# Performance work log

Measured on AMD Instinct MI355X. Metric: run time of the kernel, lower is better.

## Reference

```python
import jax, jax.numpy as jnp
import numpy as np

N = 50000      # nodes
E = 800000     # edges (before self-loops)
F_IN = 16      # input features
H = 8          # heads
C = 16         # out channels per head
HID = H * C    # 128
NEG_SLOPE = 0.2


def setup_inputs() -> dict:
    key = jax.random.key(0)
    ks = jax.random.split(key, 16)
    x = jax.random.normal(ks[0], (N, F_IN), jnp.float32)
    edge_index = jax.random.randint(ks[1], (2, E), 0, N, dtype=jnp.int64)

    def lin(k, fan_in, fan_out):
        return jax.random.normal(k, (fan_in, fan_out), jnp.float32) / np.sqrt(fan_in)

    def att(k):
        return jax.random.normal(k, (H, C), jnp.float32) * 0.1

    return {
        "x": x, "edge_index": edge_index,
        "W1": lin(ks[2], F_IN, HID), "a1_src": att(ks[3]), "a1_dst": att(ks[4]), "b1": jnp.zeros((HID,), jnp.float32),
        "W2": lin(ks[5], HID, HID),  "a2_src": att(ks[6]), "a2_dst": att(ks[7]), "b2": jnp.zeros((HID,), jnp.float32),
        "W3": lin(ks[8], HID, HID),  "a3_src": att(ks[9]), "a3_dst": att(ks[10]), "b3": jnp.zeros((HID,), jnp.float32),
        "fc_w": lin(ks[11], HID, 1), "fc_b": jnp.zeros((1,), jnp.float32),
    }


def gat_layer(x, src, dst, W, a_src, a_dst, b):
    # x: [N, Fin] -> h: [N, H, C]
    h = (x @ W).reshape(-1, H, C)
    al_src = jnp.einsum('nhc,hc->nh', h, a_src)  # [N, H]
    al_dst = jnp.einsum('nhc,hc->nh', h, a_dst)  # [N, H]
    e = jax.nn.leaky_relu(al_src[src] + al_dst[dst], NEG_SLOPE)  # [Etot, H]
    # segment softmax over destination node (self-loops guarantee nonempty segments)
    m = jax.ops.segment_max(e, dst, num_segments=N)
    p = jnp.exp(e - m[dst])
    s = jax.ops.segment_sum(p, dst, num_segments=N)
    alpha = p / s[dst]                                            # [Etot, H]
    out = jax.ops.segment_sum(h[src] * alpha[:, :, None], dst, num_segments=N)  # [N, H, C]
    return out.reshape(-1, HID) + b


def reference(x, edge_index, W1, a1_src, a1_dst, b1, W2, a2_src, a2_dst, b2,
              W3, a3_src, a3_dst, b3, fc_w, fc_b):
    loops = jnp.arange(N, dtype=edge_index.dtype)
    src = jnp.concatenate([edge_index[0], loops])  # add self-loops (PyG default)
    dst = jnp.concatenate([edge_index[1], loops])
    h = jax.nn.elu(gat_layer(x, src, dst, W1, a1_src, a1_dst, b1))
    h = jax.nn.elu(gat_layer(h, src, dst, W2, a2_src, a2_dst, b2))
    h = jax.nn.elu(gat_layer(h, src, dst, W3, a3_src, a3_dst, b3))
    return h @ fc_w + fc_b  # [N, 1]
```

## Files before the change

kernel.cpp:

```cpp
#include <hip/hip_runtime.h>
#include <math.h>

#define N_NODES 50000
#define E_EDGES 800000
#define F_IN 16
#define H_HEADS 8
#define HID 128
#define NEG_SLOPE 0.2f
#define N_PART 8
#define PART_SZ ((N_NODES + N_PART - 1) / N_PART)

typedef __attribute__((ext_vector_type(8))) short short8v;
typedef __attribute__((ext_vector_type(4))) float f32x4;

__device__ __forceinline__ unsigned short f2bf(float f) {
    unsigned u = __float_as_uint(f);
    return (unsigned short)((u + 0x7FFFu + ((u >> 16) & 1u)) >> 16);
}

__global__ void setup(int* __restrict__ deg, const float* __restrict__ W2,
                      unsigned short* __restrict__ Wt2, const float* __restrict__ W3,
                      unsigned short* __restrict__ Wt3) {
    int t = blockIdx.x * 256 + threadIdx.x;
    if (t < N_NODES) deg[t] = 0;
    if (t < HID * HID) {
        int col = t >> 7, k = t & 127;
        Wt2[t] = f2bf(W2[k * HID + col]);
        Wt3[t] = f2bf(W3[k * HID + col]);
    }
}


__global__ void hist_dst(const int* __restrict__ ei, int* __restrict__ deg) {
    int part = blockIdx.x & 7;
    int e = (blockIdx.x >> 3) * 256 + threadIdx.x;
    if (e >= E_EDGES) return;
    int d = ei[E_EDGES + e];
    if (d / PART_SZ == part) atomicAdd(&deg[d], 1);
}

__global__ void scan1(const int* __restrict__ deg, int* __restrict__ rowptr,
                      int* __restrict__ partial) {
    __shared__ int tmp[256];
    int tid = threadIdx.x;
    int t = blockIdx.x * 256 + tid;
    int v = (t < N_NODES) ? deg[t] : 0;
    tmp[tid] = v;
    __syncthreads();
    for (int off = 1; off < 256; off <<= 1) {
        int add = (tid >= off) ? tmp[tid - off] : 0;
        __syncthreads();
        tmp[tid] += add;
        __syncthreads();
    }
    if (t < N_NODES) rowptr[t] = tmp[tid] - v;
    if (tid == 255) partial[blockIdx.x] = tmp[255];
}

__global__ void scan2(int* __restrict__ partial, int nblk) {
    __shared__ int tmp[256];
    int tid = threadIdx.x;
    int v = (tid < nblk) ? partial[tid] : 0;
    tmp[tid] = v;
    __syncthreads();
    for (int off = 1; off < 256; off <<= 1) {
        int add = (tid >= off) ? tmp[tid - off] : 0;
        __syncthreads();
        tmp[tid] += add;
        __syncthreads();
    }
    if (tid < nblk) partial[tid] = tmp[tid] - v;
}

__global__ void scan3(int* __restrict__ rowptr, const int* __restrict__ partial,
                      int* __restrict__ deg) {
    int t = blockIdx.x * 256 + threadIdx.x;
    if (t < N_NODES) {
        rowptr[t] += partial[blockIdx.x];
        deg[t] = 0;
    }
    if (t == 0) rowptr[N_NODES] = E_EDGES;
}

__global__ void scatter(const int* __restrict__ ei, const int* __restrict__ rowptr,
                        int* __restrict__ cursor, int* __restrict__ csr) {
    int part = blockIdx.x & 7;
    int e = (blockIdx.x >> 3) * 256 + threadIdx.x;
    if (e >= E_EDGES) return;
    int d = ei[E_EDGES + e];
    if (d / PART_SZ != part) return;
    int s = ei[e];
    int pos = atomicAdd(&cursor[d], 1);
    csr[rowptr[d] + pos] = s;
}

template <int K>
__global__ __launch_bounds__(256) void gemm_tile(const float* __restrict__ A,
                                                 const float* __restrict__ W,
                                                 unsigned short* __restrict__ C,
                                                 const float* __restrict__ a_src,
                                                 const float* __restrict__ a_dst,
                                                 float* __restrict__ alS,
                                                 float* __restrict__ alD, int M) {
    constexpr int BK = (K < 32) ? K : 32;
    constexpr int BKQ = BK / 4;
    __shared__ float sA[BK][128];
    __shared__ float sW[BK][128];
    int tid = threadIdx.x;
    int tx = tid & 15, ty = tid >> 4;
    int row0 = blockIdx.x * 128;
    float acc[8][8] = {};

    for (int kc = 0; kc < K; kc += BK) {
#pragma unroll
        for (int f = tid; f < 128 * BKQ; f += 256) {
            int r = f / BKQ, kq = f % BKQ;
            int gr = row0 + r;
            float4 v = (gr < M) ? *(const float4*)(A + (size_t)gr * K + kc + kq * 4)
                                : make_float4(0.f, 0.f, 0.f, 0.f);
            sA[kq * 4 + 0][r] = v.x;
            sA[kq * 4 + 1][r] = v.y;
            sA[kq * 4 + 2][r] = v.z;
            sA[kq * 4 + 3][r] = v.w;
        }
#pragma unroll
        for (int f = tid; f < BK * 32; f += 256) {
            int kr = f / 32, cq = f % 32;
            *(float4*)(&sW[kr][cq * 4]) =
                *(const float4*)(W + (size_t)(kc + kr) * 128 + cq * 4);
        }
        __syncthreads();
#pragma unroll
        for (int k = 0; k < BK; k++) {
            float4 a0 = *(const float4*)(&sA[k][ty * 8]);
            float4 a1 = *(const float4*)(&sA[k][ty * 8 + 4]);
            float4 w0 = *(const float4*)(&sW[k][tx * 4]);
            float4 w1 = *(const float4*)(&sW[k][64 + tx * 4]);
            float av[8] = {a0.x, a0.y, a0.z, a0.w, a1.x, a1.y, a1.z, a1.w};
            float wv[8] = {w0.x, w0.y, w0.z, w0.w, w1.x, w1.y, w1.z, w1.w};
#pragma unroll
            for (int i = 0; i < 8; i++)
#pragma unroll
                for (int j = 0; j < 8; j++) acc[i][j] += av[i] * wv[j];
        }
        __syncthreads();
    }

    int hd0 = tx >> 2, co = (tx & 3) * 4;
    float4 as0 = *(const float4*)(a_src + hd0 * 16 + co);
    float4 as1 = *(const float4*)(a_src + (4 + hd0) * 16 + co);
    float4 ad0 = *(const float4*)(a_dst + hd0 * 16 + co);
    float4 ad1 = *(const float4*)(a_dst + (4 + hd0) * 16 + co);

#pragma unroll
    for (int i = 0; i < 8; i++) {
        int gr = row0 + ty * 8 + i;
        if (gr >= M) break;
        float4 c0 = make_float4(acc[i][0], acc[i][1], acc[i][2], acc[i][3]);
        float4 c1 = make_float4(acc[i][4], acc[i][5], acc[i][6], acc[i][7]);
        ushort4 p0 = {f2bf(c0.x), f2bf(c0.y), f2bf(c0.z), f2bf(c0.w)};
        ushort4 p1 = {f2bf(c1.x), f2bf(c1.y), f2bf(c1.z), f2bf(c1.w)};
        *(ushort4*)(C + (size_t)gr * 128 + tx * 4) = p0;
        *(ushort4*)(C + (size_t)gr * 128 + 64 + tx * 4) = p1;
        float s1a = c0.x * as0.x + c0.y * as0.y + c0.z * as0.z + c0.w * as0.w;
        float s1b = c1.x * as1.x + c1.y * as1.y + c1.z * as1.z + c1.w * as1.w;
        float s2a = c0.x * ad0.x + c0.y * ad0.y + c0.z * ad0.z + c0.w * ad0.w;
        float s2b = c1.x * ad1.x + c1.y * ad1.y + c1.z * ad1.z + c1.w * ad1.w;
        s1a += __shfl_xor(s1a, 1); s1a += __shfl_xor(s1a, 2);
        s1b += __shfl_xor(s1b, 1); s1b += __shfl_xor(s1b, 2);
        s2a += __shfl_xor(s2a, 1); s2a += __shfl_xor(s2a, 2);
        s2b += __shfl_xor(s2b, 1); s2b += __shfl_xor(s2b, 2);
        if ((tx & 3) == 0) {
            alS[gr * 8 + hd0] = s1a;
            alS[gr * 8 + 4 + hd0] = s1b;
            alD[gr * 8 + hd0] = s2a;
            alD[gr * 8 + 4 + hd0] = s2b;
        }
    }
}

__global__ __launch_bounds__(256) void gemm_mfma(const unsigned short* __restrict__ Abf,
                                                 const unsigned short* __restrict__ Wt,
                                                 unsigned short* __restrict__ C, int M) {
    __shared__ unsigned short sA[HID * HID];
    __shared__ unsigned short sW[HID * HID];
    char* sAb = (char*)sA;
    char* sWb = (char*)sW;
    int tid = threadIdx.x;
    int row0 = blockIdx.x * 128;

#pragma unroll
    for (int i = 0; i < 8; i++) {
        int f = tid + i * 256;
        int r = f >> 4, c = f & 15;
        int dst = r * 256 + ((c * 16) ^ ((r & 7) << 4));
        int gr = row0 + r;
        short8v va = {0, 0, 0, 0, 0, 0, 0, 0};
        if (gr < M) va = *(const short8v*)(Abf + (size_t)gr * HID + c * 8);
        *(short8v*)(sAb + dst) = va;
        *(short8v*)(sWb + dst) = *(const short8v*)(Wt + r * HID + c * 8);
    }
    __syncthreads();

    int lane = tid & 63;
    int wv = tid >> 6;
    int l15 = lane & 15, kg = lane >> 4;
    f32x4 acc[2][8];
#pragma unroll
    for (int a = 0; a < 2; a++)
#pragma unroll
        for (int j = 0; j < 8; j++) acc[a][j] = f32x4{0.f, 0.f, 0.f, 0.f};

    int rowA0 = wv * 32 + l15;
    int rowA1 = rowA0 + 16;
    int xr = (rowA0 & 7) << 4;

#pragma unroll
    for (int kt = 0; kt < 4; kt++) {
        int kb = kt * 64 + kg * 16;
        short8v a0 = *(const short8v*)(sAb + rowA0 * 256 + (kb ^ xr));
        short8v a1 = *(const short8v*)(sAb + rowA1 * 256 + (kb ^ xr));
#pragma unroll
        for (int j = 0; j < 8; j++) {
            int colr = j * 16 + l15;
            short8v b = *(const short8v*)(sWb + colr * 256 + (kb ^ ((colr & 7) << 4)));
            acc[0][j] = __builtin_amdgcn_mfma_f32_16x16x32_bf16(a0, b, acc[0][j], 0, 0, 0);
            acc[1][j] = __builtin_amdgcn_mfma_f32_16x16x32_bf16(a1, b, acc[1][j], 0, 0, 0);
        }
    }

#pragma unroll
    for (int a = 0; a < 2; a++) {
        int rbase = row0 + wv * 32 + a * 16 + kg * 4;
#pragma unroll
        for (int j = 0; j < 8; j++) {
            int col = j * 16 + l15;
#pragma unroll
            for (int reg = 0; reg < 4; reg++) {
                int gr = rbase + reg;
                if (gr < M) C[(size_t)gr * HID + col] = f2bf(acc[a][j][reg]);
            }
        }
    }
}

__global__ void calc_al(const unsigned short* __restrict__ hbf,
                        const float* __restrict__ a_src, const float* __restrict__ a_dst,
                        float* __restrict__ alS, float* __restrict__ alD) {
    int t = blockIdx.x * 256 + threadIdx.x;
    if (t >= N_NODES * H_HEADS) return;
    int n = t >> 3, hd = t & 7;
    const unsigned short* hr = hbf + (size_t)n * HID + hd * 16;
    float s1 = 0.f, s2 = 0.f;
#pragma unroll
    for (int c = 0; c < 16; c += 2) {
        unsigned g = *(const unsigned*)(hr + c);
        float v0 = __uint_as_float(g << 16);
        float v1 = __uint_as_float(g & 0xFFFF0000u);
        s1 += v0 * a_src[hd * 16 + c] + v1 * a_src[hd * 16 + c + 1];
        s2 += v0 * a_dst[hd * 16 + c] + v1 * a_dst[hd * 16 + c + 1];
    }
    alS[t] = s1;
    alD[t] = s2;
}

template <int MODE>
__global__ void node_agg(const int* __restrict__ rowptr, const int* __restrict__ csr,
                         const float* __restrict__ alS, const float* __restrict__ alD,
                         const unsigned short* __restrict__ hbf, const float* __restrict__ b,
                         unsigned short* __restrict__ h_out, const float* __restrict__ fcw,
                         const float* __restrict__ fcb, float* __restrict__ fco) {
    int node = blockIdx.x * 4 + (threadIdx.x >> 6);
    if (node >= N_NODES) return;
    int lane = threadIdx.x & 63;
    int row0 = __builtin_amdgcn_readfirstlane(rowptr[node]);
    int deg = __builtin_amdgcn_readfirstlane(rowptr[node + 1]) - row0;
    int h0 = lane >> 3;
    float ald = alD[node * 8 + h0];

    float es = alS[node * 8 + h0] + ald;
    es = es > 0.f ? es : NEG_SLOPE * es;
    float ps = __expf(es);
    unsigned gsl = ((const unsigned*)(hbf + (size_t)node * HID))[lane];
    float ssum = ps;
    float acc0 = ps * __uint_as_float(gsl << 16);
    float acc1 = ps * __uint_as_float(gsl & 0xFFFF0000u);

    int i = 0;
    for (; i + 16 <= deg; i += 16) {
        int su[16];
#pragma unroll
        for (int j = 0; j < 16; j++)
            su[j] = __builtin_amdgcn_readfirstlane(csr[row0 + i + j]);
        float aa[16];
        unsigned gg[16];
#pragma unroll
        for (int j = 0; j < 16; j++) {
            aa[j] = alS[su[j] * 8 + h0];
            gg[j] = ((const unsigned*)(hbf + (size_t)su[j] * HID))[lane];
        }
#pragma unroll
        for (int j = 0; j < 16; j++) {
            float e0 = aa[j] + ald;
            e0 = e0 > 0.f ? e0 : NEG_SLOPE * e0;
            float p = __expf(e0);
            ssum += p;
            acc0 += p * __uint_as_float(gg[j] << 16);
            acc1 += p * __uint_as_float(gg[j] & 0xFFFF0000u);
        }
    }
    for (; i + 4 <= deg; i += 4) {
        int su[4];
#pragma unroll
        for (int j = 0; j < 4; j++)
            su[j] = __builtin_amdgcn_readfirstlane(csr[row0 + i + j]);
        float aa[4];
        unsigned gg[4];
#pragma unroll
        for (int j = 0; j < 4; j++) {
            aa[j] = alS[su[j] * 8 + h0];
            gg[j] = ((const unsigned*)(hbf + (size_t)su[j] * HID))[lane];
        }
#pragma unroll
        for (int j = 0; j < 4; j++) {
            float e0 = aa[j] + ald;
            e0 = e0 > 0.f ? e0 : NEG_SLOPE * e0;
            float p = __expf(e0);
            ssum += p;
            acc0 += p * __uint_as_float(gg[j] << 16);
            acc1 += p * __uint_as_float(gg[j] & 0xFFFF0000u);
        }
    }
    for (; i < deg; i++) {
        int s0 = __builtin_amdgcn_readfirstlane(csr[row0 + i]);
        float a0 = alS[s0 * 8 + h0];
        unsigned g0 = ((const unsigned*)(hbf + (size_t)s0 * HID))[lane];
        float e0 = a0 + ald;
        e0 = e0 > 0.f ? e0 : NEG_SLOPE * e0;
        float p0 = __expf(e0);
        ssum += p0;
        acc0 += p0 * __uint_as_float(g0 << 16);
        acc1 += p0 * __uint_as_float(g0 & 0xFFFF0000u);
    }

    float2 bv = *(const float2*)(b + lane * 2);
    float inv = 1.f / ssum;
    float v0 = acc0 * inv + bv.x;
    float v1 = acc1 * inv + bv.y;
    v0 = v0 > 0.f ? v0 : (__expf(v0) - 1.f);
    v1 = v1 > 0.f ? v1 : (__expf(v1) - 1.f);
    if (MODE == 0) {
        unsigned pk = (unsigned)f2bf(v0) | ((unsigned)f2bf(v1) << 16);
        ((unsigned*)h_out)[(size_t)node * 64 + lane] = pk;
    } else {
        float2 fw = *(const float2*)(fcw + lane * 2);
        float r = v0 * fw.x + v1 * fw.y;
#pragma unroll
        for (int off = 32; off; off >>= 1) r += __shfl_down(r, off);
        if (lane == 0) fco[node] = r + fcb[0];
    }
}


extern "C" void kernel_launch(void* const* d_in, const int* in_sizes, int n_in,
                              void* d_out, int out_size, void* d_ws, size_t ws_size,
                              hipStream_t stream) {
    const float* x   = (const float*)d_in[0];
    const int*   ei  = (const int*)d_in[1];
    const float* W1  = (const float*)d_in[2];
    const float* a1s = (const float*)d_in[3];
    const float* a1d = (const float*)d_in[4];
    const float* b1  = (const float*)d_in[5];
    const float* W2  = (const float*)d_in[6];
    const float* a2s = (const float*)d_in[7];
    const float* a2d = (const float*)d_in[8];
    const float* b2  = (const float*)d_in[9];
    const float* W3  = (const float*)d_in[10];
    const float* a3s = (const float*)d_in[11];
    const float* a3d = (const float*)d_in[12];
    const float* b3  = (const float*)d_in[13];
    const float* fcw = (const float*)d_in[14];
    const float* fcb = (const float*)d_in[15];
    float* out = (float*)d_out;

    char* ws = (char*)d_ws;
    size_t off = 0;
    unsigned short* bufH = (unsigned short*)(ws + off); off += (size_t)N_NODES * HID * 2;
    unsigned short* bufB = (unsigned short*)(ws + off); off += (size_t)N_NODES * HID * 2;
    unsigned short* Wt2  = (unsigned short*)(ws + off); off += (size_t)HID * HID * 2;
    unsigned short* Wt3  = (unsigned short*)(ws + off); off += (size_t)HID * HID * 2;
    float* alS  = (float*)(ws + off); off += (size_t)N_NODES * H_HEADS * 4;
    float* alD  = (float*)(ws + off); off += (size_t)N_NODES * H_HEADS * 4;
    int* deg    = (int*)(ws + off);   off += (size_t)N_NODES * 4;
    int* rowptr = (int*)(ws + off);   off += (size_t)(N_NODES + 1) * 4;
    int* partial= (int*)(ws + off);   off += 256 * 4;
    int* csr    = (int*)(ws + off);   off += (size_t)E_EDGES * 4;

    const int NB_N  = (N_NODES + 255) / 256;
    const int NB_E8 = ((E_EDGES + 255) / 256) * N_PART;
    const int NB_GT = (N_NODES + 127) / 128;
    const int NB_ND = (N_NODES + 3) / 4;
    const int NB_AL = (N_NODES * H_HEADS + 255) / 256;

    setup<<<NB_N, 256, 0, stream>>>(deg, W2, Wt2, W3, Wt3);
    hist_dst<<<NB_E8, 256, 0, stream>>>(ei, deg);
    scan1<<<NB_N, 256, 0, stream>>>(deg, rowptr, partial);
    scan2<<<1, 256, 0, stream>>>(partial, NB_N);
    scan3<<<NB_N, 256, 0, stream>>>(rowptr, partial, deg);
    scatter<<<NB_E8, 256, 0, stream>>>(ei, rowptr, deg, csr);

    gemm_tile<F_IN><<<NB_GT, 256, 0, stream>>>(x, W1, bufH, a1s, a1d, alS, alD, N_NODES);
    node_agg<0><<<NB_ND, 256, 0, stream>>>(rowptr, csr, alS, alD, bufH, b1, bufB,
                                           nullptr, nullptr, nullptr);
    gemm_mfma<<<NB_GT, 256, 0, stream>>>(bufB, Wt2, bufH, N_NODES);
    calc_al<<<NB_AL, 256, 0, stream>>>(bufH, a2s, a2d, alS, alD);
    node_agg<0><<<NB_ND, 256, 0, stream>>>(rowptr, csr, alS, alD, bufH, b2, bufB,
                                           nullptr, nullptr, nullptr);
    gemm_mfma<<<NB_GT, 256, 0, stream>>>(bufB, Wt3, bufH, N_NODES);
    calc_al<<<NB_AL, 256, 0, stream>>>(bufH, a3s, a3d, alS, alD);
    node_agg<1><<<NB_ND, 256, 0, stream>>>(rowptr, csr, alS, alD, bufH, b3, nullptr,
                                           fcw, fcb, out);

    (void)in_sizes; (void)n_in; (void)out_size; (void)ws_size;
}
```

Before: 248.5 us.

## Fold attention logits into MFMA GEMM and merge small launches

Precomputes W·a_src and W·a_dst projections as an extra 16-column bf16 weight block, so the layer-2/3 MFMA GEMM emits the attention logits directly and the separate calc_al kernels go away. It also merges scan2 and scan3 into one kernel in which every block redoes the partial scan, and runs the CSR scatter and the layer-1 GEMM in a single launch split by block index. The goal is fewer kernel launches and no extra pass over the hidden features. The trade-off is that logits are now computed from bf16-rounded folded weights, which changes numerics slightly.

```diff
diff --git a/kernel.cpp b/kernel.cpp
--- a/kernel.cpp
+++ b/kernel.cpp
@@ -9,6 +9,7 @@
 #define NEG_SLOPE 0.2f
 #define N_PART 8
 #define PART_SZ ((N_NODES + N_PART - 1) / N_PART)
+#define NB_GT ((N_NODES + 127) / 128)
 
 typedef __attribute__((ext_vector_type(8))) short short8v;
 typedef __attribute__((ext_vector_type(4))) float f32x4;
@@ -18,15 +19,33 @@
     return (unsigned short)((u + 0x7FFFu + ((u >> 16) & 1u)) >> 16);
 }
 
-__global__ void setup(int* __restrict__ deg, const float* __restrict__ W2,
-                      unsigned short* __restrict__ Wt2, const float* __restrict__ W3,
-                      unsigned short* __restrict__ Wt3) {
+__global__ void setup(int* __restrict__ deg,
+                      const float* __restrict__ W2, unsigned short* __restrict__ Wt2,
+                      const float* __restrict__ W3, unsigned short* __restrict__ Wt3,
+                      const float* __restrict__ a2s, const float* __restrict__ a2d,
+                      unsigned short* __restrict__ Wal2,
+                      const float* __restrict__ a3s, const float* __restrict__ a3d,
+                      unsigned short* __restrict__ Wal3) {
     int t = blockIdx.x * 256 + threadIdx.x;
     if (t < N_NODES) deg[t] = 0;
     if (t < HID * HID) {
         int col = t >> 7, k = t & 127;
         Wt2[t] = f2bf(W2[k * HID + col]);
         Wt3[t] = f2bf(W3[k * HID + col]);
+    }
+    if (t < 16 * HID) {
+        int l = t >> 7, k = t & 127;
+        int hd = l & 7;
+        const float* av2 = (l < 8) ? a2s : a2d;
+        const float* av3 = (l < 8) ? a3s : a3d;
+        float s2 = 0.f, s3 = 0.f;
+#pragma unroll
+        for (int c = 0; c < 16; c++) {
+            s2 += W2[k * HID + hd * 16 + c] * av2[hd * 16 + c];
+            s3 += W3[k * HID + hd * 16 + c] * av3[hd * 16 + c];
+        }
+        Wal2[t] = f2bf(s2);
+        Wal3[t] = f2bf(s3);
     }
 }
 
@@ -57,7 +76,8 @@
     if (tid == 255) partial[blockIdx.x] = tmp[255];
 }
 
-__global__ void scan2(int* __restrict__ partial, int nblk) {
+__global__ void scan23(int* __restrict__ rowptr, const int* __restrict__ partial,
+                       int* __restrict__ deg, int nblk) {
     __shared__ int tmp[256];
     int tid = threadIdx.x;
     int v = (tid < nblk) ? partial[tid] : 0;
@@ -69,23 +89,24 @@
         tmp[tid] += add;
         __syncthreads();
     }
-    if (tid < nblk) partial[tid] = tmp[tid] - v;
-}
-
-__global__ void scan3(int* __restrict__ rowptr, const int* __restrict__ partial,
-                      int* __restrict__ deg) {
-    int t = blockIdx.x * 256 + threadIdx.x;
+    int incl = tmp[tid];
+    __syncthreads();
+    tmp[tid] = incl - v;
+    __syncthreads();
+    int boff = tmp[blockIdx.x];
+    int t = blockIdx.x * 256 + tid;
     if (t < N_NODES) {
-        rowptr[t] += partial[blockIdx.x];
+        rowptr[t] += boff;
         deg[t] = 0;
     }
     if (t == 0) rowptr[N_NODES] = E_EDGES;
 }
 
-__global__ void scatter(const int* __restrict__ ei, const int* __restrict__ rowptr,
-                        int* __restrict__ cursor, int* __restrict__ csr) {
-    int part = blockIdx.x & 7;
-    int e = (blockIdx.x >> 3) * 256 + threadIdx.x;
+__device__ void scatter_body(int bid, const int* __restrict__ ei,
+                             const int* __restrict__ rowptr, int* __restrict__ cursor,
+                             int* __restrict__ csr) {
+    int part = bid & 7;
+    int e = (bid >> 3) * 256 + threadIdx.x;
     if (e >= E_EDGES) return;
     int d = ei[E_EDGES + e];
     if (d / PART_SZ != part) return;
@@ -94,56 +115,54 @@
     csr[rowptr[d] + pos] = s;
 }
 
-template <int K>
-__global__ __launch_bounds__(256) void gemm_tile(const float* __restrict__ A,
-                                                 const float* __restrict__ W,
-                                                 unsigned short* __restrict__ C,
-                                                 const float* __restrict__ a_src,
-                                                 const float* __restrict__ a_dst,
-                                                 float* __restrict__ alS,
-                                                 float* __restrict__ alD, int M) {
-    constexpr int BK = (K < 32) ? K : 32;
-    constexpr int BKQ = BK / 4;
-    __shared__ float sA[BK][128];
-    __shared__ float sW[BK][128];
+__global__ __launch_bounds__(256) void scatter_gemm1(
+    const int* __restrict__ ei, const int* __restrict__ rowptr,
+    int* __restrict__ cursor, int* __restrict__ csr,
+    const float* __restrict__ A, const float* __restrict__ W,
+    unsigned short* __restrict__ C, const float* __restrict__ a_src,
+    const float* __restrict__ a_dst, float* __restrict__ alS,
+    float* __restrict__ alD) {
+    __shared__ float sA[F_IN][128];
+    __shared__ float sW[F_IN][128];
+    if (blockIdx.x >= NB_GT) {
+        scatter_body(blockIdx.x - NB_GT, ei, rowptr, cursor, csr);
+        return;
+    }
+    constexpr int K = F_IN, BKQ = F_IN / 4;
     int tid = threadIdx.x;
     int tx = tid & 15, ty = tid >> 4;
     int row0 = blockIdx.x * 128;
     float acc[8][8] = {};
 
-    for (int kc = 0; kc < K; kc += BK) {
-#pragma unroll
-        for (int f = tid; f < 128 * BKQ; f += 256) {
-            int r = f / BKQ, kq = f % BKQ;
-            int gr = row0 + r;
-            float4 v = (gr < M) ? *(const float4*)(A + (size_t)gr * K + kc + kq * 4)
-                                : make_float4(0.f, 0.f, 0.f, 0.f);
-            sA[kq * 4 + 0][r] = v.x;
-            sA[kq * 4 + 1][r] = v.y;
-            sA[kq * 4 + 2][r] = v.z;
-            sA[kq * 4 + 3][r] = v.w;
-        }
-#pragma unroll
-        for (int f = tid; f < BK * 32; f += 256) {
-            int kr = f / 32, cq = f % 32;
-            *(float4*)(&sW[kr][cq * 4]) =
-                *(const float4*)(W + (size_t)(kc + kr) * 128 + cq * 4);
-        }
-        __syncthreads();
-#pragma unroll
-        for (int k = 0; k < BK; k++) {
-            float4 a0 = *(const float4*)(&sA[k][ty * 8]);
-            float4 a1 = *(const float4*)(&sA[k][ty * 8 + 4]);
-            float4 w0 = *(const float4*)(&sW[k][tx * 4]);
-            float4 w1 = *(const float4*)(&sW[k][64 + tx * 4]);
-            float av[8] = {a0.x, a0.y, a0.z, a0.w, a1.x, a1.y, a1.z, a1.w};
-            float wv[8] = {w0.x, w0.y, w0.z, w0.w, w1.x, w1.y, w1.z, w1.w};
-#pragma unroll
-            for (int i = 0; i < 8; i++)
-#pragma unroll
-                for (int j = 0; j < 8; j++) acc[i][j] += av[i] * wv[j];
-        }
-        __syncthreads();
+#pragma unroll
+    for (int f = tid; f < 128 * BKQ; f += 256) {
+        int r = f / BKQ, kq = f % BKQ;
+        int gr = row0 + r;
+        float4 v = (gr < N_NODES) ? *(const float4*)(A + (size_t)gr * K + kq * 4)
+                                  : make_float4(0.f, 0.f, 0.f, 0.f);
+        sA[kq * 4 + 0][r] = v.x;
+        sA[kq * 4 + 1][r] = v.y;
+        sA[kq * 4 + 2][r] = v.z;
+        sA[kq * 4 + 3][r] = v.w;
+    }
+#pragma unroll
+    for (int f = tid; f < K * 32; f += 256) {
+        int kr = f / 32, cq = f % 32;
+        *(float4*)(&sW[kr][cq * 4]) = *(const float4*)(W + (size_t)kr * 128 + cq * 4);
+    }
+    __syncthreads();
+#pragma unroll
+    for (int k = 0; k < K; k++) {
+        float4 a0 = *(const float4*)(&sA[k][ty * 8]);
+        float4 a1 = *(const float4*)(&sA[k][ty * 8 + 4]);
+        float4 w0 = *(const float4*)(&sW[k][tx * 4]);
+        float4 w1 = *(const float4*)(&sW[k][64 + tx * 4]);
+        float av[8] = {a0.x, a0.y, a0.z, a0.w, a1.x, a1.y, a1.z, a1.w};
+        float wv[8] = {w0.x, w0.y, w0.z, w0.w, w1.x, w1.y, w1.z, w1.w};
+#pragma unroll
+        for (int i = 0; i < 8; i++)
+#pragma unroll
+            for (int j = 0; j < 8; j++) acc[i][j] += av[i] * wv[j];
     }
 
     int hd0 = tx >> 2, co = (tx & 3) * 4;
@@ -155,7 +174,7 @@
 #pragma unroll
     for (int i = 0; i < 8; i++) {
         int gr = row0 + ty * 8 + i;
-        if (gr >= M) break;
+        if (gr >= N_NODES) break;
         float4 c0 = make_float4(acc[i][0], acc[i][1], acc[i][2], acc[i][3]);
         float4 c1 = make_float4(acc[i][4], acc[i][5], acc[i][6], acc[i][7]);
         ushort4 p0 = {f2bf(c0.x), f2bf(c0.y), f2bf(c0.z), f2bf(c0.w)};
@@ -181,7 +200,10 @@
 
 __global__ __launch_bounds__(256) void gemm_mfma(const unsigned short* __restrict__ Abf,
                                                  const unsigned short* __restrict__ Wt,
-                                                 unsigned short* __restrict__ C, int M) {
+                                                 const unsigned short* __restrict__ Wal,
+                                                 unsigned short* __restrict__ C,
+                                                 float* __restrict__ alS,
+                                                 float* __restrict__ alD, int M) {
     __shared__ unsigned short sA[HID * HID];
     __shared__ unsigned short sW[HID * HID];
     char* sAb = (char*)sA;
@@ -200,16 +222,26 @@
         *(short8v*)(sAb + dst) = va;
         *(short8v*)(sWb + dst) = *(const short8v*)(Wt + r * HID + c * 8);
     }
-    __syncthreads();
 
     int lane = tid & 63;
     int wv = tid >> 6;
     int l15 = lane & 15, kg = lane >> 4;
+
+    short8v bal[4];
+#pragma unroll
+    for (int kt = 0; kt < 4; kt++)
+        bal[kt] = *(const short8v*)(Wal + l15 * HID + kt * 32 + kg * 8);
+
+    __syncthreads();
+
     f32x4 acc[2][8];
 #pragma unroll
     for (int a = 0; a < 2; a++)
 #pragma unroll
         for (int j = 0; j < 8; j++) acc[a][j] = f32x4{0.f, 0.f, 0.f, 0.f};
+    f32x4 aal[2];
+    aal[0] = f32x4{0.f, 0.f, 0.f, 0.f};
+    aal[1] = f32x4{0.f, 0.f, 0.f, 0.f};
 
     int rowA0 = wv * 32 + l15;
     int rowA1 = rowA0 + 16;
@@ -227,6 +259,8 @@
             acc[0][j] = __builtin_amdgcn_mfma_f32_16x16x32_bf16(a0, b, acc[0][j], 0, 0, 0);
             acc[1][j] = __builtin_amdgcn_mfma_f32_16x16x32_bf16(a1, b, acc[1][j], 0, 0, 0);
         }
+        aal[0] = __builtin_amdgcn_mfma_f32_16x16x32_bf16(a0, bal[kt], aal[0], 0, 0, 0);
+        aal[1] = __builtin_amdgcn_mfma_f32_16x16x32_bf16(a1, bal[kt], aal[1], 0, 0, 0);
     }
 
 #pragma unroll
@@ -241,27 +275,16 @@
                 if (gr < M) C[(size_t)gr * HID + col] = f2bf(acc[a][j][reg]);
             }
         }
-    }
-}
-
-__global__ void calc_al(const unsigned short* __restrict__ hbf,
-                        const float* __restrict__ a_src, const float* __restrict__ a_dst,
-                        float* __restrict__ alS, float* __restrict__ alD) {
-    int t = blockIdx.x * 256 + threadIdx.x;
-    if (t >= N_NODES * H_HEADS) return;
-    int n = t >> 3, hd = t & 7;
-    const unsigned short* hr = hbf + (size_t)n * HID + hd * 16;
-    float s1 = 0.f, s2 = 0.f;
-#pragma unroll
-    for (int c = 0; c < 16; c += 2) {
-        unsigned g = *(const unsigned*)(hr + c);
-        float v0 = __uint_as_float(g << 16);
-        float v1 = __uint_as_float(g & 0xFFFF0000u);
-        s1 += v0 * a_src[hd * 16 + c] + v1 * a_src[hd * 16 + c + 1];
-        s2 += v0 * a_dst[hd * 16 + c] + v1 * a_dst[hd * 16 + c + 1];
-    }
-    alS[t] = s1;
-    alD[t] = s2;
+#pragma unroll
+        for (int reg = 0; reg < 4; reg++) {
+            int gr = rbase + reg;
+            if (gr < M) {
+                float v = aal[a][reg];
+                if (l15 < 8) alS[gr * 8 + l15] = v;
+                else alD[gr * 8 + (l15 - 8)] = v;
+            }
+        }
+    }
 }
 
 template <int MODE>
@@ -389,6 +412,8 @@
     unsigned short* bufB = (unsigned short*)(ws + off); off += (size_t)N_NODES * HID * 2;
     unsigned short* Wt2  = (unsigned short*)(ws + off); off += (size_t)HID * HID * 2;
     unsigned short* Wt3  = (unsigned short*)(ws + off); off += (size_t)HID * HID * 2;
+    unsigned short* Wal2 = (unsigned short*)(ws + off); off += (size_t)16 * HID * 2;
+    unsigned short* Wal3 = (unsigned short*)(ws + off); off += (size_t)16 * HID * 2;
     float* alS  = (float*)(ws + off); off += (size_t)N_NODES * H_HEADS * 4;
     float* alD  = (float*)(ws + off); off += (size_t)N_NODES * H_HEADS * 4;
     int* deg    = (int*)(ws + off);   off += (size_t)N_NODES * 4;
@@ -398,26 +423,21 @@
 
     const int NB_N  = (N_NODES + 255) / 256;
     const int NB_E8 = ((E_EDGES + 255) / 256) * N_PART;
-    const int NB_GT = (N_NODES + 127) / 128;
     const int NB_ND = (N_NODES + 3) / 4;
-    const int NB_AL = (N_NODES * H_HEADS + 255) / 256;
-
-    setup<<<NB_N, 256, 0, stream>>>(deg, W2, Wt2, W3, Wt3);
+
+    setup<<<NB_N, 256, 0, stream>>>(deg, W2, Wt2, W3, Wt3, a2s, a2d, Wal2, a3s, a3d, Wal3);
     hist_dst<<<NB_E8, 256, 0, stream>>>(ei, deg);
     scan1<<<NB_N, 256, 0, stream>>>(deg, rowptr, partial);
-    scan2<<<1, 256, 0, stream>>>(partial, NB_N);
-    scan3<<<NB_N, 256, 0, stream>>>(rowptr, partial, deg);
-    scatter<<<NB_E8, 256, 0, stream>>>(ei, rowptr, deg, csr);
-
-    gemm_tile<F_IN><<<NB_GT, 256, 0, stream>>>(x, W1, bufH, a1s, a1d, alS, alD, N_NODES);
+    scan23<<<NB_N, 256, 0, stream>>>(rowptr, partial, deg, NB_N);
+
+    scatter_gemm1<<<NB_GT + NB_E8, 256, 0, stream>>>(ei, rowptr, deg, csr,
+                                                     x, W1, bufH, a1s, a1d, alS, alD);
     node_agg<0><<<NB_ND, 256, 0, stream>>>(rowptr, csr, alS, alD, bufH, b1, bufB,
                                            nullptr, nullptr, nullptr);
-    gemm_mfma<<<NB_GT, 256, 0, stream>>>(bufB, Wt2, bufH, N_NODES);
-    calc_al<<<NB_AL, 256, 0, stream>>>(bufH, a2s, a2d, alS, alD);
+    gemm_mfma<<<NB_GT, 256, 0, stream>>>(bufB, Wt2, Wal2, bufH, alS, alD, N_NODES);
     node_agg<0><<<NB_ND, 256, 0, stream>>>(rowptr, csr, alS, alD, bufH, b2, bufB,
                                            nullptr, nullptr, nullptr);
-    gemm_mfma<<<NB_GT, 256, 0, stream>>>(bufB, Wt3, bufH, N_NODES);
-    calc_al<<<NB_AL, 256, 0, stream>>>(bufH, a3s, a3d, alS, alD);
+    gemm_mfma<<<NB_GT, 256, 0, stream>>>(bufB, Wt3, Wal3, bufH, alS, alD, N_NODES);
     node_agg<1><<<NB_ND, 256, 0, stream>>>(rowptr, csr, alS, alD, bufH, b3, nullptr,
                                            fcw, fcb, out);
 
```

New measurement: 285.3 us. +14.8%, slower.
